# Optimization experiments

Measured on AMD Instinct MI355X. Metric: run time of the kernel, lower is better.

## Reference

```python
import jax, jax.numpy as jnp
import numpy as np

N_NODES = 50000
N_HEADS = 8


def _make_edges(n, e_rand, seed=0):
    # unique random edges + self-loops so every row has >=1 neighbor
    rng = np.random.default_rng(seed)
    flat = rng.integers(0, n * n, size=e_rand, dtype=np.int64)
    flat = np.unique(np.concatenate([flat, np.arange(n, dtype=np.int64) * (n + 1)]))
    src = (flat // n).astype(np.int32)
    dst = (flat % n).astype(np.int32)
    return jnp.stack([jnp.asarray(src), jnp.asarray(dst)])


def setup_inputs() -> dict:
    key = jax.random.key(0)
    ks = jax.random.split(key, 10)
    d_in, d_att, d_out = 256, 64, 256
    dph = d_out // N_HEADS  # 32, per-head output dim of linearW
    s = 0.05
    return {
        "features": jax.random.normal(ks[0], (N_NODES, d_in), jnp.float32),
        "edge_index": _make_edges(N_NODES, 1_600_000),
        "Wq": jax.random.normal(ks[1], (N_HEADS, d_att, d_in), jnp.float32) * s,
        "bq": jax.random.normal(ks[2], (N_HEADS, d_att), jnp.float32) * s,
        "Wk": jax.random.normal(ks[3], (N_HEADS, d_att, d_in), jnp.float32) * s,
        "bk": jax.random.normal(ks[4], (N_HEADS, d_att), jnp.float32) * s,
        "Ww": jax.random.normal(ks[5], (dph, d_in), jnp.float32) * s,
        "bw": jax.random.normal(ks[6], (dph,), jnp.float32) * s,
        "Wb": jax.random.normal(ks[7], (d_out, d_in), jnp.float32) * s,
        "bb": jax.random.normal(ks[8], (d_out,), jnp.float32) * s,
    }


def reference(features, edge_index, Wq, bq, Wk, bk, Ww, bw, Wb, bb):
    n = features.shape[0]
    src, dst = edge_index[0], edge_index[1]
    # shared value projection (linearW is one layer reused for all heads)
    V = features @ Ww.T + bw  # [N, dph]
    head_outs = []
    for h in range(N_HEADS):  # structural loop over heads, as in the original
        q = features @ Wq[h].T + bq[h]  # [N, d_att]
        k = features @ Wk[h].T + bk[h]  # [N, d_att]
        s = jnp.sum(q[src] * k[dst], axis=-1)  # [E] = scores[i,j]=q_i.k_j on edges
        # row-wise (per source node) softmax over neighbors == dense masked softmax
        smax = jax.ops.segment_max(s, src, num_segments=n)
        ex = jnp.exp(s - jax.lax.stop_gradient(smax)[src])
        denom = jax.ops.segment_sum(ex, src, num_segments=n)
        alpha = ex / denom[src]  # [E]
        head_outs.append(jax.ops.segment_sum(alpha[:, None] * V[dst], src, num_segments=n))
    agg = jnp.concatenate(head_outs, axis=1)  # [N, d_out]
    return features @ Wb.T + bb + agg
```

## Files before the change

### kernel.cpp

```cpp
#include <hip/hip_runtime.h>
#include <hip/hip_fp16.h>

typedef _Float16 f16;
typedef _Float16 f16x2 __attribute__((ext_vector_type(2)));
typedef _Float16 f16x8 __attribute__((ext_vector_type(8)));
typedef float f32x4 __attribute__((ext_vector_type(4)));

#define WC_ROWS 1312
#define WC_PAD 1408

__global__ void prep_weights(const float* __restrict__ Wq, const float* __restrict__ bq,
                             const float* __restrict__ Wk, const float* __restrict__ bk,
                             const float* __restrict__ Ww, const float* __restrict__ bw,
                             const float* __restrict__ Wb, const float* __restrict__ bb,
                             f16* __restrict__ Wc, float* __restrict__ bias) {
    int id = blockIdx.x * 256 + threadIdx.x;
    int j = id >> 8, k = id & 255;
    if (j >= WC_PAD) return;
    float v;
    if (j < 512)       v = Wq[j*256 + k];
    else if (j < 1024) v = Wk[(j-512)*256 + k];
    else if (j < 1056) v = Ww[(j-1024)*256 + k];
    else if (j < 1312) v = Wb[(j-1056)*256 + k];
    else               v = 0.f;
    Wc[j*256 + k] = (f16)v;
    if (k == 0) {
        float b;
        if (j < 512)       b = bq[j];
        else if (j < 1024) b = bk[j-512];
        else if (j < 1056) b = bw[j-1024];
        else if (j < 1312) b = bb[j-1056];
        else               b = 0.f;
        bias[j] = b;
    }
}

__global__ void build_rows(const int* __restrict__ src, int E, int n, int* __restrict__ rs) {
    int e = blockIdx.x * 256 + threadIdx.x;
    if (e == 0) rs[n] = E;
    if (e < E) {
        if (e == 0 || src[e] != src[e-1]) rs[src[e]] = e;
    }
}

__device__ __forceinline__ int swz_slot(int row, int c) {
    return row * 4 + (c ^ (row & 3) ^ ((row >> 2) & 3));
}

__device__ __forceinline__ uint4 cvt8(float4 a, float4 b) {
    f16x8 o;
    o[0] = (f16)a.x; o[1] = (f16)a.y; o[2] = (f16)a.z; o[3] = (f16)a.w;
    o[4] = (f16)b.x; o[5] = (f16)b.y; o[6] = (f16)b.z; o[7] = (f16)b.w;
    return __builtin_bit_cast(uint4, o);
}

__launch_bounds__(256)
__global__ void gemm_fused(const float* __restrict__ F, const f16* __restrict__ Wc,
                           const float* __restrict__ bias,
                           f16* __restrict__ Qb, f16* __restrict__ Kb, f16* __restrict__ Vb,
                           float* __restrict__ Out, int n) {
    __shared__ uint4 As4[512];
    __shared__ uint4 Bs4[512];
    int t = threadIdx.x;
    int lane = t & 63, w = t >> 6;
    int wm = w >> 1, wn = w & 1;
    long m0 = (long)blockIdx.y * 128;
    int n0 = blockIdx.x * 128;

    f32x4 acc[4][4];
    #pragma unroll
    for (int i = 0; i < 4; i++)
        #pragma unroll
        for (int j = 0; j < 4; j++)
            acc[i][j] = (f32x4){0.f, 0.f, 0.f, 0.f};

    int lrow = t >> 2, lc = t & 3;
    long row0 = m0 + lrow, row1 = m0 + 64 + lrow;
    const float4* Fg0 = (const float4*)(F + row0 * 256 + lc * 8);
    const float4* Fg1 = (const float4*)(F + row1 * 256 + lc * 8);
    const uint4*  Bg0 = (const uint4*)(Wc + (long)(n0 + lrow) * 256 + lc * 8);
    const uint4*  Bg1 = (const uint4*)(Wc + (long)(n0 + 64 + lrow) * 256 + lc * 8);
    bool ok0 = row0 < n, ok1 = row1 < n;
    int ws0 = swz_slot(lrow, lc);
    int ws1 = swz_slot(lrow + 64, lc);
    int csw = (lane >> 4) ^ (lane & 3) ^ ((lane >> 2) & 3);
    int arow = wm * 64 + (lane & 15);
    int brow = wn * 64 + (lane & 15);

    float4 fa0 = {}, fb0 = {}, fa1 = {}, fb1 = {};
    if (ok0) { fa0 = Fg0[0]; fb0 = Fg0[1]; }
    if (ok1) { fa1 = Fg1[0]; fb1 = Fg1[1]; }
    uint4 rb0 = Bg0[0], rb1 = Bg1[0];
    for (int kt = 0; kt < 8; ++kt) {
        if (kt) __syncthreads();
        As4[ws0] = cvt8(fa0, fb0);
        As4[ws1] = cvt8(fa1, fb1);
        Bs4[ws0] = rb0;
        Bs4[ws1] = rb1;
        __syncthreads();
        if (kt < 7) {
            if (ok0) { fa0 = Fg0[(kt + 1) * 8]; fb0 = Fg0[(kt + 1) * 8 + 1]; }
            if (ok1) { fa1 = Fg1[(kt + 1) * 8]; fb1 = Fg1[(kt + 1) * 8 + 1]; }
            rb0 = Bg0[(kt + 1) * 4];
            rb1 = Bg1[(kt + 1) * 4];
        }
        f16x8 af[4], bf[4];
        const f16x8* Ap = (const f16x8*)As4;
        const f16x8* Bp = (const f16x8*)Bs4;
        #pragma unroll
        for (int i = 0; i < 4; i++) af[i] = Ap[(arow + i * 16) * 4 + csw];
        #pragma unroll
        for (int j = 0; j < 4; j++) bf[j] = Bp[(brow + j * 16) * 4 + csw];
        #pragma unroll
        for (int i = 0; i < 4; i++)
            #pragma unroll
            for (int j = 0; j < 4; j++)
                acc[i][j] = __builtin_amdgcn_mfma_f32_16x16x32_f16(af[i], bf[j], acc[i][j], 0, 0, 0);
    }

    #pragma unroll
    for (int i = 0; i < 4; i++) {
        long gmb = m0 + wm * 64 + i * 16 + (lane >> 4) * 4;
        #pragma unroll
        for (int j = 0; j < 4; j++) {
            int gn = n0 + wn * 64 + j * 16 + (lane & 15);
            float bv = bias[gn];
            #pragma unroll
            for (int r = 0; r < 4; r++) {
                long gm = gmb + r;
                if (gm >= n) continue;
                float v = acc[i][j][r] + bv;
                if (gn < 512)       Qb[gm * 512 + gn] = (f16)v;
                else if (gn < 1024) Kb[gm * 512 + (gn - 512)] = (f16)v;
                else if (gn < 1056) Vb[gm * 32 + (gn - 1024)] = (f16)v;
                else if (gn < 1312) Out[gm * 256 + (gn - 1056)] = v;
            }
        }
    }
}

__device__ __forceinline__ float fd2(unsigned a, unsigned b, float c) {
#if defined(__has_builtin)
#if __has_builtin(__builtin_amdgcn_fdot2)
    return __builtin_amdgcn_fdot2(__builtin_bit_cast(f16x2, a), __builtin_bit_cast(f16x2, b), c, false);
#else
    f16x2 x = __builtin_bit_cast(f16x2, a), y = __builtin_bit_cast(f16x2, b);
    return c + (float)x[0] * (float)y[0] + (float)x[1] * (float)y[1];
#endif
#else
    f16x2 x = __builtin_bit_cast(f16x2, a), y = __builtin_bit_cast(f16x2, b);
    return c + (float)x[0] * (float)y[0] + (float)x[1] * (float)y[1];
#endif
}

__launch_bounds__(256)
__global__ void edge_scores(const int* __restrict__ srcA, const int* __restrict__ dstA,
                            const f16* __restrict__ Qb, const f16* __restrict__ Kb,
                            f16* __restrict__ sE, int E, int Epad) {
    int bid = blockIdx.x;
    int h = bid & 7;
    int j = threadIdx.x & 7;
    int g = threadIdx.x >> 3;
    int e0 = (bid >> 3) * 128 + g;
    int s[4], d[4];
    #pragma unroll
    for (int u = 0; u < 4; u++) {
        int e = e0 + 32 * u;
        bool ok = e < E;
        s[u] = ok ? srcA[e] : 0;
        d[u] = ok ? dstA[e] : 0;
    }
    uint4 kv[4], qv[4];
    #pragma unroll
    for (int u = 0; u < 4; u++)
        kv[u] = *(const uint4*)(Kb + (size_t)d[u] * 512 + h * 64 + j * 8);
    #pragma unroll
    for (int u = 0; u < 4; u++)
        qv[u] = *(const uint4*)(Qb + (size_t)s[u] * 512 + h * 64 + j * 8);
    float aa[4];
    #pragma unroll
    for (int u = 0; u < 4; u++) {
        float a = 0.f;
        a = fd2(qv[u].x, kv[u].x, a);
        a = fd2(qv[u].y, kv[u].y, a);
        a = fd2(qv[u].z, kv[u].z, a);
        a = fd2(qv[u].w, kv[u].w, a);
        aa[u] = a;
    }
    f16x2 p01, p23;
    p01[0] = (f16)aa[0]; p01[1] = (f16)aa[1];
    p23[0] = (f16)aa[2]; p23[1] = (f16)aa[3];
    unsigned u01 = __builtin_bit_cast(unsigned, p01);
    unsigned u23 = __builtin_bit_cast(unsigned, p23);
    #pragma unroll
    for (int off = 1; off < 8; off <<= 1) {
        unsigned v01 = __shfl_xor(u01, off);
        unsigned v23 = __shfl_xor(u23, off);
        f16x2 r01 = __builtin_bit_cast(f16x2, u01) + __builtin_bit_cast(f16x2, v01);
        f16x2 r23 = __builtin_bit_cast(f16x2, u23) + __builtin_bit_cast(f16x2, v23);
        u01 = __builtin_bit_cast(unsigned, r01);
        u23 = __builtin_bit_cast(unsigned, r23);
    }
    if (j == 0) {
        f16x2 r01 = __builtin_bit_cast(f16x2, u01);
        f16x2 r23 = __builtin_bit_cast(f16x2, u23);
        size_t bo = (size_t)h * Epad;
        if (e0 < E)      sE[bo + e0]      = r01[0];
        if (e0+32 < E)   sE[bo + e0+32]   = r01[1];
        if (e0+64 < E)   sE[bo + e0+64]   = r23[0];
        if (e0+96 < E)   sE[bo + e0+96]   = r23[1];
    }
}

__launch_bounds__(256)
__global__ void transpose_sE(const f16* __restrict__ sE, f16* __restrict__ sT,
                             int E, int Epad) {
    long e8 = (long)blockIdx.x * 2048 + (long)threadIdx.x * 8;
    if (e8 >= E) return;
    f16x8 rowv[8];
    #pragma unroll
    for (int h = 0; h < 8; h++)
        rowv[h] = *(const f16x8*)(sE + (size_t)h * Epad + e8);
    #pragma unroll
    for (int u = 0; u < 8; u++) {
        long e = e8 + u;
        if (e < E) {
            f16x8 o;
            #pragma unroll
            for (int h = 0; h < 8; h++) o[h] = rowv[h][u];
            *(f16x8*)(sT + (size_t)e * 8) = o;
        }
    }
}

__launch_bounds__(256)
__global__ void edge_agg(const int* __restrict__ rs, const int* __restrict__ dstA,
                         const f16* __restrict__ sT, const f16* __restrict__ Vb,
                         float* __restrict__ Out, int n) {
    __shared__ __align__(16) f16 P_lds[4][16][64];
    __shared__ int dS[4][64];
    int w = threadIdx.x >> 6, lane = threadIdx.x & 63;
    int row = blockIdx.x * 4 + w;
    if (row >= n) return;
    int e0 = rs[row], deg = rs[row + 1] - e0;
    {
        f16x8 z = {};
        *(f16x8*)&P_lds[w][8 + (lane >> 3)][(lane & 7) * 8] = z;
    }
    asm volatile("" ::: "memory");
    float m[8];
    #pragma unroll
    for (int h = 0; h < 8; h++) m[h] = -1e30f;
    f32x4 acc0 = {}, acc1 = {}, accl = {};
    int ec0 = (lane >> 4) * 8, h_a = lane & 15, hsel = (lane >> 4) & 1;
    f16x8 ones;
    #pragma unroll
    for (int j = 0; j < 8; j++) ones[j] = (f16)1.f;

    for (int base = 0; base < deg; base += 64) {
        int nE = deg - base; if (nE > 64) nE = 64;
        bool act = lane < nE;
        int ee = e0 + base + (act ? lane : 0);
        dS[w][lane] = dstA[ee];
        f16x8 s8 = *(const f16x8*)(sT + (size_t)ee * 8);
        f16x2 mx[4];
        #pragma unroll
        for (int p = 0; p < 4; p++) {
            f16x2 v;
            v[0] = s8[2*p]; v[1] = s8[2*p + 1];
            if (!act) { v[0] = (f16)(-65504.f); v[1] = (f16)(-65504.f); }
            mx[p] = v;
        }
        #pragma unroll
        for (int off = 1; off < 64; off <<= 1) {
            #pragma unroll
            for (int p = 0; p < 4; p++) {
                unsigned o = __shfl_xor(__builtin_bit_cast(unsigned, mx[p]), off);
                mx[p] = __builtin_elementwise_max(mx[p], __builtin_bit_cast(f16x2, o));
            }
        }
        float sc[8];
        #pragma unroll
        for (int h = 0; h < 8; h++) {
            float tv = (float)mx[h >> 1][h & 1];
            float nm = fmaxf(m[h], tv);
            sc[h] = __expf(m[h] - nm);
            float sv = act ? (float)s8[h] : -1e30f;
            float p = act ? __expf(sv - nm) : 0.f;
            P_lds[w][h][lane ^ (h << 3)] = (f16)p;
            m[h] = nm;
        }
        #pragma unroll
        for (int r = 0; r < 4; r++) {
            float f = hsel ? sc[r + 4] : sc[r];
            acc0[r] *= f;
            acc1[r] *= f;
            accl[r] *= f;
        }
        asm volatile("" ::: "memory");
        f16x8 a0 = *(const f16x8*)&P_lds[w][h_a][(ec0)      ^ ((h_a & 7) << 3)];
        f16x8 a1 = *(const f16x8*)&P_lds[w][h_a][(32 + ec0) ^ ((h_a & 7) << 3)];
        f16x8 bf0a, bf0b, bf1a, bf1b;
        #pragma unroll
        for (int j = 0; j < 8; j++) {
            int dd0 = dS[w][ec0 + j];
            int dd1 = dS[w][32 + ec0 + j];
            const f16* vp0 = Vb + (size_t)dd0 * 32 + (lane & 15);
            const f16* vp1 = Vb + (size_t)dd1 * 32 + (lane & 15);
            bf0a[j] = vp0[0];  bf0b[j] = vp0[16];
            bf1a[j] = vp1[0];  bf1b[j] = vp1[16];
        }
        asm volatile("" ::: "memory");
        acc0 = __builtin_amdgcn_mfma_f32_16x16x32_f16(a0, bf0a, acc0, 0, 0, 0);
        acc0 = __builtin_amdgcn_mfma_f32_16x16x32_f16(a1, bf1a, acc0, 0, 0, 0);
        acc1 = __builtin_amdgcn_mfma_f32_16x16x32_f16(a0, bf0b, acc1, 0, 0, 0);
        acc1 = __builtin_amdgcn_mfma_f32_16x16x32_f16(a1, bf1b, acc1, 0, 0, 0);
        accl = __builtin_amdgcn_mfma_f32_16x16x32_f16(a0, ones, accl, 0, 0, 0);
        accl = __builtin_amdgcn_mfma_f32_16x16x32_f16(a1, ones, accl, 0, 0, 0);
    }
    if (lane < 32) {
        float* op = Out + (size_t)row * 256 + (lane & 15);
        #pragma unroll
        for (int r = 0; r < 4; r++) {
            int h = hsel * 4 + r;
            float inv = 1.f / accl[r];
            op[h * 32]      += acc0[r] * inv;
            op[h * 32 + 16] += acc1[r] * inv;
        }
    }
}

extern "C" void kernel_launch(void* const* d_in, const int* in_sizes, int n_in,
                              void* d_out, int out_size, void* d_ws, size_t ws_size,
                              hipStream_t stream) {
    const float* F  = (const float*)d_in[0];
    const int*   ei = (const int*)d_in[1];
    const float* Wq = (const float*)d_in[2];
    const float* bq = (const float*)d_in[3];
    const float* Wk = (const float*)d_in[4];
    const float* bk = (const float*)d_in[5];
    const float* Ww = (const float*)d_in[6];
    const float* bw = (const float*)d_in[7];
    const float* Wb = (const float*)d_in[8];
    const float* bb = (const float*)d_in[9];
    int n = in_sizes[0] / 256;
    int E = in_sizes[1] / 2;
    const int* srcA = ei;
    const int* dstA = ei + E;
    int n_pad = (n + 127) & ~127;
    int Epad = (E + 63) & ~63;

    char* wp = (char*)d_ws;
    auto alloc = [&](size_t bytes) { void* p = wp; wp += (bytes + 255) & ~255ull; return p; };
    f16*   sE   = (f16*)alloc((size_t)Epad * 8 * 2);
    f16*   Wc   = (f16*)alloc((size_t)WC_PAD * 256 * 2);
    float* bias = (float*)alloc((size_t)WC_PAD * 4);
    f16*   Qb   = (f16*)alloc((size_t)n * 512 * 2);
    f16*   Kb   = (f16*)alloc((size_t)n * 512 * 2);
    f16*   Vb   = (f16*)alloc((size_t)n * 32 * 2);
    int*   rs   = (int*)alloc((size_t)(n + 1) * 4);
    float* Out  = (float*)d_out;
    f16*   sT   = Qb;

    prep_weights<<<WC_PAD, 256, 0, stream>>>(Wq, bq, Wk, bk, Ww, bw, Wb, bb, Wc, bias);
    build_rows<<<(E + 255) / 256, 256, 0, stream>>>(srcA, E, n, rs);
    dim3 g(WC_PAD / 128, n_pad / 128);
    gemm_fused<<<g, 256, 0, stream>>>(F, Wc, bias, Qb, Kb, Vb, Out, n);
    int wgph = (E + 127) / 128;
    edge_scores<<<8 * wgph, 256, 0, stream>>>(srcA, dstA, Qb, Kb, sE, E, Epad);
    transpose_sE<<<(int)((E + 2047) / 2048), 256, 0, stream>>>(sE, sT, E, Epad);
    edge_agg<<<(n + 3) / 4, 256, 0, stream>>>(rs, dstA, sT, Vb, Out, n);
}
```

Measured before the change: 425.8 us.

## Pre-convert features to fp16 and double-buffer GEMM tiles via direct global-to-LDS loads

Adds a separate kernel that converts the fp32 feature matrix to fp16 (zero-padded to the tile multiple) in a workspace region shared with the edge-score buffer. The fused projection GEMM then loads both operands with global_load_lds straight into a double-buffered, XOR-swizzled LDS tile, prefetching the next K-slice while MFMAs run on the current one, and drops one barrier per iteration. This removes per-block fp32 loads and in-register conversion, which were repeated across the 11 column blocks. The cost is an extra pass over the features (read fp32, write fp16), and the aliasing of the fp16 features with sE assumes the GEMM finishes before edge_scores writes.

```diff
diff --git a/kernel.cpp b/kernel.cpp
--- a/kernel.cpp
+++ b/kernel.cpp
@@ -3,6 +3,7 @@
 
 typedef _Float16 f16;
 typedef _Float16 f16x2 __attribute__((ext_vector_type(2)));
+typedef _Float16 f16x4v __attribute__((ext_vector_type(4)));
 typedef _Float16 f16x8 __attribute__((ext_vector_type(8)));
 typedef float f32x4 __attribute__((ext_vector_type(4)));
 
@@ -35,6 +36,18 @@
     }
 }
 
+__global__ void conv_feat(const float* __restrict__ F, f16* __restrict__ Fh,
+                          int n, long total) {
+    long id = (long)blockIdx.x * 256 + threadIdx.x;
+    long base = id * 4;
+    if (base >= total) return;
+    long row = base >> 8;
+    float4 v = make_float4(0.f, 0.f, 0.f, 0.f);
+    if (row < n) v = *(const float4*)(F + base);
+    f16x4v o = { (f16)v.x, (f16)v.y, (f16)v.z, (f16)v.w };
+    *(f16x4v*)(Fh + base) = o;
+}
+
 __global__ void build_rows(const int* __restrict__ src, int E, int n, int* __restrict__ rs) {
     int e = blockIdx.x * 256 + threadIdx.x;
     if (e == 0) rs[n] = E;
@@ -43,24 +56,21 @@
     }
 }
 
-__device__ __forceinline__ int swz_slot(int row, int c) {
-    return row * 4 + (c ^ (row & 3) ^ ((row >> 2) & 3));
-}
-
-__device__ __forceinline__ uint4 cvt8(float4 a, float4 b) {
-    f16x8 o;
-    o[0] = (f16)a.x; o[1] = (f16)a.y; o[2] = (f16)a.z; o[3] = (f16)a.w;
-    o[4] = (f16)b.x; o[5] = (f16)b.y; o[6] = (f16)b.z; o[7] = (f16)b.w;
-    return __builtin_bit_cast(uint4, o);
+__device__ __forceinline__ int frow(int r) { return (r & 3) ^ ((r >> 2) & 3); }
+
+__device__ __forceinline__ void gload16(const f16* g, f16* l) {
+    __builtin_amdgcn_global_load_lds(
+        (const __attribute__((address_space(1))) void*)g,
+        (__attribute__((address_space(3))) void*)l, 16, 0, 0);
 }
 
 __launch_bounds__(256)
-__global__ void gemm_fused(const float* __restrict__ F, const f16* __restrict__ Wc,
+__global__ void gemm_fused(const f16* __restrict__ A, const f16* __restrict__ Wc,
                            const float* __restrict__ bias,
                            f16* __restrict__ Qb, f16* __restrict__ Kb, f16* __restrict__ Vb,
                            float* __restrict__ Out, int n) {
-    __shared__ uint4 As4[512];
-    __shared__ uint4 Bs4[512];
+    __shared__ uint4 As4[2][512];
+    __shared__ uint4 Bs4[2][512];
     int t = threadIdx.x;
     int lane = t & 63, w = t >> 6;
     int wm = w >> 1, wn = w & 1;
@@ -75,38 +85,36 @@
             acc[i][j] = (f32x4){0.f, 0.f, 0.f, 0.f};
 
     int lrow = t >> 2, lc = t & 3;
-    long row0 = m0 + lrow, row1 = m0 + 64 + lrow;
-    const float4* Fg0 = (const float4*)(F + row0 * 256 + lc * 8);
-    const float4* Fg1 = (const float4*)(F + row1 * 256 + lc * 8);
-    const uint4*  Bg0 = (const uint4*)(Wc + (long)(n0 + lrow) * 256 + lc * 8);
-    const uint4*  Bg1 = (const uint4*)(Wc + (long)(n0 + 64 + lrow) * 256 + lc * 8);
-    bool ok0 = row0 < n, ok1 = row1 < n;
-    int ws0 = swz_slot(lrow, lc);
-    int ws1 = swz_slot(lrow + 64, lc);
+    int cs = lc ^ frow(lrow);
+    const f16* Ag0 = A + (m0 + lrow) * 256 + cs * 8;
+    const f16* Ag1 = A + (m0 + 64 + lrow) * 256 + cs * 8;
+    const f16* Bg0 = Wc + (long)(n0 + lrow) * 256 + cs * 8;
+    const f16* Bg1 = Wc + (long)(n0 + 64 + lrow) * 256 + cs * 8;
+    f16* ldsA0 = (f16*)&As4[0][w * 64];
+    f16* ldsA1 = (f16*)&As4[0][256 + w * 64];
+    f16* ldsB0 = (f16*)&Bs4[0][w * 64];
+    f16* ldsB1 = (f16*)&Bs4[0][256 + w * 64];
+
     int csw = (lane >> 4) ^ (lane & 3) ^ ((lane >> 2) & 3);
     int arow = wm * 64 + (lane & 15);
     int brow = wn * 64 + (lane & 15);
 
-    float4 fa0 = {}, fb0 = {}, fa1 = {}, fb1 = {};
-    if (ok0) { fa0 = Fg0[0]; fb0 = Fg0[1]; }
-    if (ok1) { fa1 = Fg1[0]; fb1 = Fg1[1]; }
-    uint4 rb0 = Bg0[0], rb1 = Bg1[0];
+    #define STAGE(kt, b)  do {                              \
+        int ko = (kt) * 32, bo = (b) * 512 * 8;             \
+        gload16(Ag0 + ko, ldsA0 + bo);                      \
+        gload16(Ag1 + ko, ldsA1 + bo);                      \
+        gload16(Bg0 + ko, ldsB0 + bo);                      \
+        gload16(Bg1 + ko, ldsB1 + bo);                      \
+    } while (0)
+
+    STAGE(0, 0);
     for (int kt = 0; kt < 8; ++kt) {
-        if (kt) __syncthreads();
-        As4[ws0] = cvt8(fa0, fb0);
-        As4[ws1] = cvt8(fa1, fb1);
-        Bs4[ws0] = rb0;
-        Bs4[ws1] = rb1;
+        int b = kt & 1;
         __syncthreads();
-        if (kt < 7) {
-            if (ok0) { fa0 = Fg0[(kt + 1) * 8]; fb0 = Fg0[(kt + 1) * 8 + 1]; }
-            if (ok1) { fa1 = Fg1[(kt + 1) * 8]; fb1 = Fg1[(kt + 1) * 8 + 1]; }
-            rb0 = Bg0[(kt + 1) * 4];
-            rb1 = Bg1[(kt + 1) * 4];
-        }
+        if (kt < 7) STAGE(kt + 1, b ^ 1);
         f16x8 af[4], bf[4];
-        const f16x8* Ap = (const f16x8*)As4;
-        const f16x8* Bp = (const f16x8*)Bs4;
+        const f16x8* Ap = (const f16x8*)As4[b];
+        const f16x8* Bp = (const f16x8*)Bs4[b];
         #pragma unroll
         for (int i = 0; i < 4; i++) af[i] = Ap[(arow + i * 16) * 4 + csw];
         #pragma unroll
@@ -117,6 +125,7 @@
             for (int j = 0; j < 4; j++)
                 acc[i][j] = __builtin_amdgcn_mfma_f32_16x16x32_f16(af[i], bf[j], acc[i][j], 0, 0, 0);
     }
+    #undef STAGE
 
     #pragma unroll
     for (int i = 0; i < 4; i++) {
@@ -352,7 +361,11 @@
 
     char* wp = (char*)d_ws;
     auto alloc = [&](size_t bytes) { void* p = wp; wp += (bytes + 255) & ~255ull; return p; };
-    f16*   sE   = (f16*)alloc((size_t)Epad * 8 * 2);
+    size_t fhB = (size_t)n_pad * 256 * 2;
+    size_t seB = (size_t)Epad * 8 * 2;
+    void*  reg0 = alloc(fhB > seB ? fhB : seB);
+    f16*   Fh   = (f16*)reg0;
+    f16*   sE   = (f16*)reg0;
     f16*   Wc   = (f16*)alloc((size_t)WC_PAD * 256 * 2);
     float* bias = (float*)alloc((size_t)WC_PAD * 4);
     f16*   Qb   = (f16*)alloc((size_t)n * 512 * 2);
@@ -363,9 +376,11 @@
     f16*   sT   = Qb;
 
     prep_weights<<<WC_PAD, 256, 0, stream>>>(Wq, bq, Wk, bk, Ww, bw, Wb, bb, Wc, bias);
+    long totalF = (long)n_pad * 256;
+    conv_feat<<<(int)((totalF / 4 + 255) / 256), 256, 0, stream>>>(F, Fh, n, totalF);
     build_rows<<<(E + 255) / 256, 256, 0, stream>>>(srcA, E, n, rs);
     dim3 g(WC_PAD / 128, n_pad / 128);
-    gemm_fused<<<g, 256, 0, stream>>>(F, Wc, bias, Qb, Kb, Vb, Out, n);
+    gemm_fused<<<g, 256, 0, stream>>>(Fh, Wc, bias, Qb, Kb, Vb, Out, n);
     int wgph = (E + 127) / 128;
     edge_scores<<<8 * wgph, 256, 0, stream>>>(srcA, dstA, Qb, Kb, sE, E, Epad);
     transpose_sE<<<(int)((E + 2047) / 2048), 256, 0, stream>>>(sE, sT, E, Epad);
```

New measurement: 419.5 us. About the same (-1.5%).
